# Kernel tuning notes

Hardware: AMD Instinct MI355X
Metric: run time of the kernel (lower is better)

Reference implementation:

```python
import jax, jax.numpy as jnp
import numpy as np

NEG_INF = -1.0e9
LEAKY_SLOPE = 0.2


def setup_inputs() -> dict:
    key = jax.random.key(0)
    k_h, k_w, k_wb, k_a, k_ab, k_m = jax.random.split(key, 6)
    B, S, N, F_in, F_out = 4, 256, 128, 128, 128
    h = jax.random.normal(k_h, (B, S, N, F_in), dtype=jnp.float32)
    # Linear(in_features, out_features): W_w [F_in, F_out], W_b [F_out]
    lim_w = 1.0 / np.sqrt(F_in)
    W_w = jax.random.uniform(k_w, (F_in, F_out), jnp.float32, -lim_w, lim_w)
    W_b = jax.random.uniform(k_wb, (F_out,), jnp.float32, -lim_w, lim_w)
    # Linear(2*F_out, 1): split the weight into a1 (acts on Wh_i) and a2 (acts on Wh_j)
    lim_a = 1.0 / np.sqrt(2 * F_out)
    a_full = jax.random.uniform(k_a, (2 * F_out,), jnp.float32, -lim_a, lim_a)
    a1, a2 = a_full[:F_out], a_full[F_out:]
    a_b = jax.random.uniform(k_ab, (), jnp.float32, -lim_a, lim_a)
    adj_mask = jax.random.randint(k_m, (N, N), 0, 2, dtype=jnp.int32)
    return {"h": h, "W_w": W_w, "W_b": W_b, "a1": a1, "a2": a2,
            "a_b": a_b, "adj_mask": adj_mask}


def reference(h, W_w, W_b, a1, a2, a_b, adj_mask):
    # h: [B, S, N, F_in]
    Wh = jnp.einsum('bsnf,fg->bsng', h, W_w) + W_b          # [B,S,N,F_out]
    # e_ij = leakyrelu(a . [Wh_i ; Wh_j] + b) = leakyrelu(f1_i + f2_j + b)
    f1 = jnp.einsum('bsng,g->bsn', Wh, a1)                   # row term
    f2 = jnp.einsum('bsng,g->bsn', Wh, a2)                   # col term
    e = jax.nn.leaky_relu(f1[..., :, None] + f2[..., None, :] + a_b,
                          negative_slope=LEAKY_SLOPE)        # [B,S,N,N]
    e = jnp.where(adj_mask == 0, NEG_INF, e)
    attention = jax.nn.softmax(e, axis=-1)
    # dropout is identity in eval mode (deterministic reference)
    h_prime = jnp.einsum('bsij,bsjg->bsig', attention, Wh)   # [B,S,N,F_out]
    return jax.nn.elu(h_prime)
```

## Files before the change

kernel.cpp:

```cpp
#include <hip/hip_runtime.h>
#include <hip/hip_bf16.h>
#include <cmath>

namespace {

typedef __attribute__((ext_vector_type(8))) short bf16x8;
typedef __attribute__((ext_vector_type(4))) float f32x4;

constexpr float kNegInf = -1000000000.0f;
constexpr float kSlope  = 0.2f;
constexpr float kLog2e  = 1.44269504088896340736f;

__device__ __forceinline__ unsigned short f2bf(float x) {
  unsigned int u = __float_as_uint(x);
  u = (u + 0x7FFFu + ((u >> 16) & 1u)) >> 16;
  return (unsigned short)u;
}
__device__ __forceinline__ unsigned int f2bf2(float a, float b) {
  __hip_bfloat162 t = __float22bfloat162_rn(float2{a, b});
  union { __hip_bfloat162 h; unsigned int u; } c;
  c.h = t;
  return c.u;
}
__device__ __forceinline__ float exp2_hw(float x) {
#if __has_builtin(__builtin_amdgcn_exp2f)
  return __builtin_amdgcn_exp2f(x);
#else
  float r;
  asm("v_exp_f32 %0, %1\n\ts_nop 1" : "=v"(r) : "v"(x));
  return r;
#endif
}


__global__ void prep1(const float* __restrict__ Ww, const float* __restrict__ Wb,
                      const float* __restrict__ a1v, const float* __restrict__ a2v,
                      float* __restrict__ wa1, float* __restrict__ wa2,
                      float* __restrict__ ba) {
  const int k = threadIdx.x;
  if (k < 128) {
    float s1 = 0.f, s2 = 0.f;
    for (int g = 0; g < 128; ++g) {
      const float w = Ww[k * 128 + g];
      s1 = fmaf(w, a1v[g], s1);
      s2 = fmaf(w, a2v[g], s2);
    }
    wa1[k] = s1 * kLog2e;
    wa2[k] = s2 * kLog2e;
  }
  if (k == 128) {
    float s1 = 0.f, s2 = 0.f;
    for (int g = 0; g < 128; ++g) {
      s1 = fmaf(Wb[g], a1v[g], s1);
      s2 = fmaf(Wb[g], a2v[g], s2);
    }
    ba[0] = s1 * kLog2e;
    ba[1] = s2 * kLog2e;
  }
}

__global__ void prep2(const float* __restrict__ Ww, const int* __restrict__ adj,
                      const float* __restrict__ wa1, const float* __restrict__ wa2,
                      unsigned short* __restrict__ wf, unsigned int* __restrict__ adjp) {
  const int tid = blockIdx.x * 256 + threadIdx.x;
  if (tid < 18432) {
    const int j = tid & 7, l = (tid >> 3) & 63, kc = (tid >> 9) & 3, g = tid >> 11;
    const int k = kc * 32 + ((l >> 4) << 3) + j;
    const int c = l & 15;
    float x;
    if (g < 8) x = Ww[k * 128 + g * 16 + c];
    else       x = (c == 0) ? wa1[k] : (c == 1) ? wa2[k] : 0.f;
    wf[tid] = f2bf(x);
  }
  if (tid < 512) {
    const int row = tid >> 2, wd = tid & 3;
    const int* ap = adj + row * 128 + wd * 32;
    unsigned int bits = 0u;
#pragma unroll
    for (int b = 0; b < 32; ++b) bits |= (ap[b] != 0 ? (1u << b) : 0u);
    adjp[tid] = bits;
  }
}

struct SMemA {
  unsigned short Whs[8][4][64][8];
  float f1s[128];
  float f2s[128];
  unsigned int adjs[512];
};
union SMemU {
  SMemA a;
  float stage[4][16][132];
};

__global__ __launch_bounds__(256, 4) void gat_mfma(
    const float* __restrict__ h,
    const float* __restrict__ Wb,
    const float* __restrict__ abp,
    const unsigned short* __restrict__ wf,
    const unsigned int* __restrict__ adjp,
    const float* __restrict__ ba,
    float* __restrict__ out) {
  __shared__ SMemU smu;
  SMemA& sm = smu.a;
  const int t    = threadIdx.x;
  const int lane = t & 63;
  const int w    = t >> 6;
  const int lr   = lane & 15;
  const int lg   = lane >> 4;
  const int bs   = blockIdx.x;
  const float ab2 = abp[0] * kLog2e;

  *(uint2*)(sm.adjs + t * 2) = *(const uint2*)(adjp + t * 2);

  const float* hblk = h + (size_t)bs * 16384;
  const int R0 = w * 32;

  bf16x8 ha[2][4];
#pragma unroll
  for (int rt = 0; rt < 2; ++rt)
#pragma unroll
    for (int kc = 0; kc < 4; ++kc) {
      const float* p = hblk + (R0 + rt * 16 + lr) * 128 + kc * 32 + lg * 8;
      f32x4 v0 = *(const f32x4*)p;
      f32x4 v1 = *(const f32x4*)(p + 4);
      union { bf16x8 v; unsigned int u[4]; } pk;
      pk.u[0] = f2bf2(v0[0], v0[1]);
      pk.u[1] = f2bf2(v0[2], v0[3]);
      pk.u[2] = f2bf2(v1[0], v1[1]);
      pk.u[3] = f2bf2(v1[2], v1[3]);
      ha[rt][kc] = pk.v;
    }

  f32x4 acc[2][9];
#pragma unroll
  for (int rt = 0; rt < 2; ++rt)
#pragma unroll
    for (int g = 0; g < 9; ++g) acc[rt][g] = (f32x4){0.f, 0.f, 0.f, 0.f};

#pragma unroll
  for (int g = 0; g < 9; ++g)
#pragma unroll
    for (int kc = 0; kc < 4; ++kc) {
      const bf16x8 bh = *(const bf16x8*)(wf + ((g * 4 + kc) * 64 + lane) * 8);
      acc[0][g] = __builtin_amdgcn_mfma_f32_16x16x32_bf16(ha[0][kc], bh, acc[0][g], 0, 0, 0);
      acc[1][g] = __builtin_amdgcn_mfma_f32_16x16x32_bf16(ha[1][kc], bh, acc[1][g], 0, 0, 0);
    }

  float wbc[8];
#pragma unroll
  for (int g = 0; g < 8; ++g) wbc[g] = Wb[g * 16 + lr];
  const float ba1 = ba[0], ba2 = ba[1];

#pragma unroll
  for (int rt = 0; rt < 2; ++rt) {
#pragma unroll
    for (int r = 0; r < 4; ++r) {
#pragma unroll
      for (int g = 0; g < 8; ++g) acc[rt][g][r] += wbc[g];
      const int row = R0 + rt * 16 + lg * 4 + r;
      if (lr == 0)      sm.f1s[row] = acc[rt][8][r] + ba1;
      else if (lr == 1) sm.f2s[row] = acc[rt][8][r] + ba2;
    }
#pragma unroll
    for (int g = 0; g < 8; ++g) {
      const unsigned int plo = f2bf2(acc[rt][g][0], acc[rt][g][1]);
      const unsigned int phi = f2bf2(acc[rt][g][2], acc[rt][g][3]);
      const int lp = (2 * rt + (lg >> 1)) * 16 + lr;
      const int jb = (lg & 1) * 4;
      *(uint2*)(&sm.Whs[g][w][lp][jb]) = make_uint2(plo, phi);
    }
  }
  __syncthreads();

  bf16x8 af[2][4];
  float s0 = 0.f, s1 = 0.f;
  const float f1i0 = sm.f1s[R0 + lr] + ab2;
  const float f1i1 = sm.f1s[R0 + 16 + lr] + ab2;
  const int rq0 = (R0 + lr) * 4, rq1 = (R0 + 16 + lr) * 4;
#pragma unroll
  for (int kc = 0; kc < 4; ++kc) {
    const f32x4 fv0 = *(const f32x4*)(&sm.f2s[kc * 32 + lg * 8]);
    const f32x4 fv1 = *(const f32x4*)(&sm.f2s[kc * 32 + lg * 8 + 4]);
    const unsigned int aw0 = sm.adjs[rq0 + kc];
    const unsigned int aw1 = sm.adjs[rq1 + kc];
    union { bf16x8 v; unsigned int u[4]; } pk0, pk1;
#pragma unroll
    for (int qq = 0; qq < 4; ++qq) {
      float e0[2], e1[2];
#pragma unroll
      for (int hh = 0; hh < 2; ++hh) {
        const int q = qq * 2 + hh;
        const float fj = (q < 4) ? fv0[q] : fv1[q - 4];
        const unsigned int bit = 1u << (lg * 8 + q);
        float x0 = f1i0 + fj;
        x0 = x0 >= 0.f ? x0 : kSlope * x0;
        x0 = (aw0 & bit) ? x0 : kNegInf;
        e0[hh] = exp2_hw(x0);
        float x1 = f1i1 + fj;
        x1 = x1 >= 0.f ? x1 : kSlope * x1;
        x1 = (aw1 & bit) ? x1 : kNegInf;
        e1[hh] = exp2_hw(x1);
      }
      const unsigned int u0 = f2bf2(e0[0], e0[1]);
      const unsigned int u1 = f2bf2(e1[0], e1[1]);
      pk0.u[qq] = u0;
      pk1.u[qq] = u1;
      s0 += __uint_as_float(u0 << 16) + __uint_as_float(u0 & 0xffff0000u);
      s1 += __uint_as_float(u1 << 16) + __uint_as_float(u1 & 0xffff0000u);
    }
    af[0][kc] = pk0.v;
    af[1][kc] = pk1.v;
  }
  s0 += __shfl_xor(s0, 16);
  s0 += __shfl_xor(s0, 32);
  s1 += __shfl_xor(s1, 16);
  s1 += __shfl_xor(s1, 32);
  float rs[2] = {s0, s1};

  f32x4 acc2[2][8];
#pragma unroll
  for (int rt = 0; rt < 2; ++rt)
#pragma unroll
    for (int g = 0; g < 8; ++g) acc2[rt][g] = (f32x4){0.f, 0.f, 0.f, 0.f};

#pragma unroll
  for (int g = 0; g < 8; ++g)
#pragma unroll
    for (int kc = 0; kc < 4; ++kc) {
      const bf16x8 bw = *(const bf16x8*)(&sm.Whs[g][kc][lane][0]);
      acc2[0][g] = __builtin_amdgcn_mfma_f32_16x16x32_bf16(af[0][kc], bw, acc2[0][g], 0, 0, 0);
      acc2[1][g] = __builtin_amdgcn_mfma_f32_16x16x32_bf16(af[1][kc], bw, acc2[1][g], 0, 0, 0);
    }
  __syncthreads();

  float* oblk = out + (size_t)bs * 16384;
#pragma unroll
  for (int rt = 0; rt < 2; ++rt) {
    float inv[4];
#pragma unroll
    for (int r = 0; r < 4; ++r) {
      const float lsum = __shfl(rs[rt], (lane & 48) | (lg * 4 + r));
      inv[r] = __builtin_amdgcn_rcpf(lsum);
    }
#pragma unroll
    for (int r = 0; r < 4; ++r)
#pragma unroll
      for (int g = 0; g < 8; ++g) {
        float v = acc2[rt][g][r] * inv[r];
        v = v > 0.f ? v : __expf(v) - 1.0f;
        smu.stage[w][lg * 4 + r][g * 16 + lr] = v;
      }
#pragma unroll
    for (int sstep = 0; sstep < 8; ++sstep) {
      const int row16 = ((sstep & 1) << 3) + (lane >> 3);
      const int cd    = ((sstep >> 1) << 5) + ((lane & 7) << 2);
      f32x4 vv = *(const f32x4*)(&smu.stage[w][row16][cd]);
      *(f32x4*)(oblk + (size_t)(R0 + rt * 16 + row16) * 128 + cd) = vv;
    }
  }
}

}

extern "C" void kernel_launch(void* const* d_in, const int* in_sizes, int n_in,
                              void* d_out, int out_size, void* d_ws, size_t ws_size,
                              hipStream_t stream) {
  const float* h   = (const float*)d_in[0];
  const float* Ww  = (const float*)d_in[1];
  const float* Wb  = (const float*)d_in[2];
  const float* a1v = (const float*)d_in[3];
  const float* a2v = (const float*)d_in[4];
  const float* ab  = (const float*)d_in[5];
  const int*   adj = (const int*)d_in[6];
  float* out = (float*)d_out;

  unsigned short* wf   = (unsigned short*)d_ws;
  unsigned int*   adjp = (unsigned int*)((char*)d_ws + 36864);
  float*          wa1  = (float*)((char*)d_ws + 38912);
  float*          wa2  = (float*)((char*)d_ws + 39424);
  float*          ba   = (float*)((char*)d_ws + 39936);

  hipLaunchKernelGGL(prep1, dim3(1), dim3(256), 0, stream, Ww, Wb, a1v, a2v, wa1, wa2, ba);
  hipLaunchKernelGGL(prep2, dim3(72), dim3(256), 0, stream, Ww, adj, wa1, wa2, wf, adjp);

  const int BS = in_sizes[0] / 16384;
  hipLaunchKernelGGL(gat_mfma, dim3(BS), dim3(256), 0, stream,
                     h, Wb, ab, wf, adjp, ba, out);
}
```

Baseline: 47.83 us.

## Split fused GAT kernel into separate GEMM and attention kernels via workspace

Splits the single fused kernel into two. The first computes Wh in bf16 plus the f1/f2 row and column terms and writes them to a global workspace. The second reads them back to do the masked softmax, the aggregation MFMA and the ELU. This drops the mid-kernel barrier and the large LDS footprint, which could raise occupancy. The cost is an extra launch and a global round trip of about 2 MB of Wh. The fused path is kept as a fallback when the workspace is too small.

```diff
diff --git a/kernel.cpp b/kernel.cpp
--- a/kernel.cpp
+++ b/kernel.cpp
@@ -32,6 +32,8 @@
 #endif
 }
 
+constexpr size_t kOffF  = 40960;
+constexpr size_t kOffWh = 1089536;
 
 __global__ void prep1(const float* __restrict__ Ww, const float* __restrict__ Wb,
                       const float* __restrict__ a1v, const float* __restrict__ a2v,
@@ -82,37 +84,13 @@
   }
 }
 
-struct SMemA {
-  unsigned short Whs[8][4][64][8];
-  float f1s[128];
-  float f2s[128];
-  unsigned int adjs[512];
-};
-union SMemU {
-  SMemA a;
-  float stage[4][16][132];
-};
-
-__global__ __launch_bounds__(256, 4) void gat_mfma(
-    const float* __restrict__ h,
-    const float* __restrict__ Wb,
-    const float* __restrict__ abp,
-    const unsigned short* __restrict__ wf,
-    const unsigned int* __restrict__ adjp,
-    const float* __restrict__ ba,
-    float* __restrict__ out) {
-  __shared__ SMemU smu;
-  SMemA& sm = smu.a;
-  const int t    = threadIdx.x;
-  const int lane = t & 63;
-  const int w    = t >> 6;
-  const int lr   = lane & 15;
-  const int lg   = lane >> 4;
-  const int bs   = blockIdx.x;
-  const float ab2 = abp[0] * kLog2e;
-
-  *(uint2*)(sm.adjs + t * 2) = *(const uint2*)(adjp + t * 2);
-
+__global__ __launch_bounds__(256, 4) void gat_gemm1(
+    const float* __restrict__ h, const float* __restrict__ Wb,
+    const unsigned short* __restrict__ wf, const float* __restrict__ ba,
+    unsigned short* __restrict__ wsWh, float* __restrict__ wsF) {
+  const int t = threadIdx.x, lane = t & 63, w = t >> 6;
+  const int lr = lane & 15, lg = lane >> 4;
+  const int bs = blockIdx.x;
   const float* hblk = h + (size_t)bs * 16384;
   const int R0 = w * 32;
 
@@ -151,6 +129,8 @@
 #pragma unroll
   for (int g = 0; g < 8; ++g) wbc[g] = Wb[g * 16 + lr];
   const float ba1 = ba[0], ba2 = ba[1];
+  unsigned short* whb = wsWh + (size_t)bs * 16384;
+  float* fb = wsF + bs * 256;
 
 #pragma unroll
   for (int rt = 0; rt < 2; ++rt) {
@@ -159,8 +139,8 @@
 #pragma unroll
       for (int g = 0; g < 8; ++g) acc[rt][g][r] += wbc[g];
       const int row = R0 + rt * 16 + lg * 4 + r;
-      if (lr == 0)      sm.f1s[row] = acc[rt][8][r] + ba1;
-      else if (lr == 1) sm.f2s[row] = acc[rt][8][r] + ba2;
+      if (lr == 0)      fb[row]       = acc[rt][8][r] + ba1;
+      else if (lr == 1) fb[128 + row] = acc[rt][8][r] + ba2;
     }
 #pragma unroll
     for (int g = 0; g < 8; ++g) {
@@ -168,22 +148,35 @@
       const unsigned int phi = f2bf2(acc[rt][g][2], acc[rt][g][3]);
       const int lp = (2 * rt + (lg >> 1)) * 16 + lr;
       const int jb = (lg & 1) * 4;
-      *(uint2*)(&sm.Whs[g][w][lp][jb]) = make_uint2(plo, phi);
-    }
-  }
-  __syncthreads();
+      *(uint2*)(whb + ((g * 4 + w) * 64 + lp) * 8 + jb) = make_uint2(plo, phi);
+    }
+  }
+}
+
+__global__ __launch_bounds__(256, 4) void gat_attn(
+    const unsigned short* __restrict__ wsWh, const float* __restrict__ wsF,
+    const unsigned int* __restrict__ adjp, const float* __restrict__ abp,
+    float* __restrict__ out) {
+  __shared__ float stage[4][16][132];
+  const int t = threadIdx.x, lane = t & 63, w = t >> 6;
+  const int lr = lane & 15, lg = lane >> 4;
+  const int bs = blockIdx.x;
+  const float ab2 = abp[0] * kLog2e;
+  const float* fb = wsF + bs * 256;
+  const unsigned short* whb = wsWh + (size_t)bs * 16384;
+  const int R0 = w * 32;
 
   bf16x8 af[2][4];
   float s0 = 0.f, s1 = 0.f;
-  const float f1i0 = sm.f1s[R0 + lr] + ab2;
-  const float f1i1 = sm.f1s[R0 + 16 + lr] + ab2;
+  const float f1i0 = fb[R0 + lr] + ab2;
+  const float f1i1 = fb[R0 + 16 + lr] + ab2;
   const int rq0 = (R0 + lr) * 4, rq1 = (R0 + 16 + lr) * 4;
 #pragma unroll
   for (int kc = 0; kc < 4; ++kc) {
-    const f32x4 fv0 = *(const f32x4*)(&sm.f2s[kc * 32 + lg * 8]);
-    const f32x4 fv1 = *(const f32x4*)(&sm.f2s[kc * 32 + lg * 8 + 4]);
-    const unsigned int aw0 = sm.adjs[rq0 + kc];
-    const unsigned int aw1 = sm.adjs[rq1 + kc];
+    const f32x4 fv0 = *(const f32x4*)(fb + 128 + kc * 32 + lg * 8);
+    const f32x4 fv1 = *(const f32x4*)(fb + 128 + kc * 32 + lg * 8 + 4);
+    const unsigned int aw0 = adjp[rq0 + kc];
+    const unsigned int aw1 = adjp[rq1 + kc];
     union { bf16x8 v; unsigned int u[4]; } pk0, pk1;
 #pragma unroll
     for (int qq = 0; qq < 4; ++qq) {
@@ -228,6 +221,178 @@
   for (int g = 0; g < 8; ++g)
 #pragma unroll
     for (int kc = 0; kc < 4; ++kc) {
+      const bf16x8 bw = *(const bf16x8*)(whb + ((g * 4 + kc) * 64 + lane) * 8);
+      acc2[0][g] = __builtin_amdgcn_mfma_f32_16x16x32_bf16(af[0][kc], bw, acc2[0][g], 0, 0, 0);
+      acc2[1][g] = __builtin_amdgcn_mfma_f32_16x16x32_bf16(af[1][kc], bw, acc2[1][g], 0, 0, 0);
+    }
+
+  float* oblk = out + (size_t)bs * 16384;
+#pragma unroll
+  for (int rt = 0; rt < 2; ++rt) {
+    float inv[4];
+#pragma unroll
+    for (int r = 0; r < 4; ++r) {
+      const float lsum = __shfl(rs[rt], (lane & 48) | (lg * 4 + r));
+      inv[r] = __builtin_amdgcn_rcpf(lsum);
+    }
+#pragma unroll
+    for (int r = 0; r < 4; ++r)
+#pragma unroll
+      for (int g = 0; g < 8; ++g) {
+        float v = acc2[rt][g][r] * inv[r];
+        v = v > 0.f ? v : __expf(v) - 1.0f;
+        stage[w][lg * 4 + r][g * 16 + lr] = v;
+      }
+#pragma unroll
+    for (int sstep = 0; sstep < 8; ++sstep) {
+      const int row16 = ((sstep & 1) << 3) + (lane >> 3);
+      const int cd    = ((sstep >> 1) << 5) + ((lane & 7) << 2);
+      f32x4 vv = *(const f32x4*)(&stage[w][row16][cd]);
+      *(f32x4*)(oblk + (size_t)(R0 + rt * 16 + row16) * 128 + cd) = vv;
+    }
+  }
+}
+
+struct SMemA {
+  unsigned short Whs[8][4][64][8];
+  float f1s[128];
+  float f2s[128];
+  unsigned int adjs[512];
+};
+union SMemU {
+  SMemA a;
+  float stage[4][16][132];
+};
+
+__global__ __launch_bounds__(256, 4) void gat_mfma(
+    const float* __restrict__ h, const float* __restrict__ Wb,
+    const float* __restrict__ abp, const unsigned short* __restrict__ wf,
+    const unsigned int* __restrict__ adjp, const float* __restrict__ ba,
+    float* __restrict__ out) {
+  __shared__ SMemU smu;
+  SMemA& sm = smu.a;
+  const int t = threadIdx.x, lane = t & 63, w = t >> 6;
+  const int lr = lane & 15, lg = lane >> 4;
+  const int bs = blockIdx.x;
+  const float ab2 = abp[0] * kLog2e;
+
+  *(uint2*)(sm.adjs + t * 2) = *(const uint2*)(adjp + t * 2);
+
+  const float* hblk = h + (size_t)bs * 16384;
+  const int R0 = w * 32;
+
+  bf16x8 ha[2][4];
+#pragma unroll
+  for (int rt = 0; rt < 2; ++rt)
+#pragma unroll
+    for (int kc = 0; kc < 4; ++kc) {
+      const float* p = hblk + (R0 + rt * 16 + lr) * 128 + kc * 32 + lg * 8;
+      f32x4 v0 = *(const f32x4*)p;
+      f32x4 v1 = *(const f32x4*)(p + 4);
+      union { bf16x8 v; unsigned int u[4]; } pk;
+      pk.u[0] = f2bf2(v0[0], v0[1]);
+      pk.u[1] = f2bf2(v0[2], v0[3]);
+      pk.u[2] = f2bf2(v1[0], v1[1]);
+      pk.u[3] = f2bf2(v1[2], v1[3]);
+      ha[rt][kc] = pk.v;
+    }
+
+  f32x4 acc[2][9];
+#pragma unroll
+  for (int rt = 0; rt < 2; ++rt)
+#pragma unroll
+    for (int g = 0; g < 9; ++g) acc[rt][g] = (f32x4){0.f, 0.f, 0.f, 0.f};
+
+#pragma unroll
+  for (int g = 0; g < 9; ++g)
+#pragma unroll
+    for (int kc = 0; kc < 4; ++kc) {
+      const bf16x8 bh = *(const bf16x8*)(wf + ((g * 4 + kc) * 64 + lane) * 8);
+      acc[0][g] = __builtin_amdgcn_mfma_f32_16x16x32_bf16(ha[0][kc], bh, acc[0][g], 0, 0, 0);
+      acc[1][g] = __builtin_amdgcn_mfma_f32_16x16x32_bf16(ha[1][kc], bh, acc[1][g], 0, 0, 0);
+    }
+
+  float wbc[8];
+#pragma unroll
+  for (int g = 0; g < 8; ++g) wbc[g] = Wb[g * 16 + lr];
+  const float ba1 = ba[0], ba2 = ba[1];
+
+#pragma unroll
+  for (int rt = 0; rt < 2; ++rt) {
+#pragma unroll
+    for (int r = 0; r < 4; ++r) {
+#pragma unroll
+      for (int g = 0; g < 8; ++g) acc[rt][g][r] += wbc[g];
+      const int row = R0 + rt * 16 + lg * 4 + r;
+      if (lr == 0)      sm.f1s[row] = acc[rt][8][r] + ba1;
+      else if (lr == 1) sm.f2s[row] = acc[rt][8][r] + ba2;
+    }
+#pragma unroll
+    for (int g = 0; g < 8; ++g) {
+      const unsigned int plo = f2bf2(acc[rt][g][0], acc[rt][g][1]);
+      const unsigned int phi = f2bf2(acc[rt][g][2], acc[rt][g][3]);
+      const int lp = (2 * rt + (lg >> 1)) * 16 + lr;
+      const int jb = (lg & 1) * 4;
+      *(uint2*)(&sm.Whs[g][w][lp][jb]) = make_uint2(plo, phi);
+    }
+  }
+  __syncthreads();
+
+  bf16x8 af[2][4];
+  float s0 = 0.f, s1 = 0.f;
+  const float f1i0 = sm.f1s[R0 + lr] + ab2;
+  const float f1i1 = sm.f1s[R0 + 16 + lr] + ab2;
+  const int rq0 = (R0 + lr) * 4, rq1 = (R0 + 16 + lr) * 4;
+#pragma unroll
+  for (int kc = 0; kc < 4; ++kc) {
+    const f32x4 fv0 = *(const f32x4*)(&sm.f2s[kc * 32 + lg * 8]);
+    const f32x4 fv1 = *(const f32x4*)(&sm.f2s[kc * 32 + lg * 8 + 4]);
+    const unsigned int aw0 = sm.adjs[rq0 + kc];
+    const unsigned int aw1 = sm.adjs[rq1 + kc];
+    union { bf16x8 v; unsigned int u[4]; } pk0, pk1;
+#pragma unroll
+    for (int qq = 0; qq < 4; ++qq) {
+      float e0[2], e1[2];
+#pragma unroll
+      for (int hh = 0; hh < 2; ++hh) {
+        const int q = qq * 2 + hh;
+        const float fj = (q < 4) ? fv0[q] : fv1[q - 4];
+        const unsigned int bit = 1u << (lg * 8 + q);
+        float x0 = f1i0 + fj;
+        x0 = x0 >= 0.f ? x0 : kSlope * x0;
+        x0 = (aw0 & bit) ? x0 : kNegInf;
+        e0[hh] = exp2_hw(x0);
+        float x1 = f1i1 + fj;
+        x1 = x1 >= 0.f ? x1 : kSlope * x1;
+        x1 = (aw1 & bit) ? x1 : kNegInf;
+        e1[hh] = exp2_hw(x1);
+      }
+      const unsigned int u0 = f2bf2(e0[0], e0[1]);
+      const unsigned int u1 = f2bf2(e1[0], e1[1]);
+      pk0.u[qq] = u0;
+      pk1.u[qq] = u1;
+      s0 += __uint_as_float(u0 << 16) + __uint_as_float(u0 & 0xffff0000u);
+      s1 += __uint_as_float(u1 << 16) + __uint_as_float(u1 & 0xffff0000u);
+    }
+    af[0][kc] = pk0.v;
+    af[1][kc] = pk1.v;
+  }
+  s0 += __shfl_xor(s0, 16);
+  s0 += __shfl_xor(s0, 32);
+  s1 += __shfl_xor(s1, 16);
+  s1 += __shfl_xor(s1, 32);
+  float rs[2] = {s0, s1};
+
+  f32x4 acc2[2][8];
+#pragma unroll
+  for (int rt = 0; rt < 2; ++rt)
+#pragma unroll
+    for (int g = 0; g < 8; ++g) acc2[rt][g] = (f32x4){0.f, 0.f, 0.f, 0.f};
+
+#pragma unroll
+  for (int g = 0; g < 8; ++g)
+#pragma unroll
+    for (int kc = 0; kc < 4; ++kc) {
       const bf16x8 bw = *(const bf16x8*)(&sm.Whs[g][kc][lane][0]);
       acc2[0][g] = __builtin_amdgcn_mfma_f32_16x16x32_bf16(af[0][kc], bw, acc2[0][g], 0, 0, 0);
       acc2[1][g] = __builtin_amdgcn_mfma_f32_16x16x32_bf16(af[1][kc], bw, acc2[1][g], 0, 0, 0);
@@ -281,10 +446,18 @@
   float*          wa2  = (float*)((char*)d_ws + 39424);
   float*          ba   = (float*)((char*)d_ws + 39936);
 
+  const int BS = in_sizes[0] / 16384;
+  const size_t need = kOffWh + (size_t)BS * 16384 * sizeof(unsigned short);
+
   hipLaunchKernelGGL(prep1, dim3(1), dim3(256), 0, stream, Ww, Wb, a1v, a2v, wa1, wa2, ba);
   hipLaunchKernelGGL(prep2, dim3(72), dim3(256), 0, stream, Ww, adj, wa1, wa2, wf, adjp);
 
-  const int BS = in_sizes[0] / 16384;
-  hipLaunchKernelGGL(gat_mfma, dim3(BS), dim3(256), 0, stream,
-                     h, Wb, ab, wf, adjp, ba, out);
-}
+  if (ws_size >= need) {
+    float*          wsF  = (float*)((char*)d_ws + kOffF);
+    unsigned short* wsWh = (unsigned short*)((char*)d_ws + kOffWh);
+    hipLaunchKernelGGL(gat_gemm1, dim3(BS), dim3(256), 0, stream, h, Wb, wf, ba, wsWh, wsF);
+    hipLaunchKernelGGL(gat_attn, dim3(BS), dim3(256), 0, stream, wsWh, wsF, adjp, ab, out);
+  } else {
+    hipLaunchKernelGGL(gat_mfma, dim3(BS), dim3(256), 0, stream, h, Wb, ab, wf, adjp, ba, out);
+  }
+}
```

Measured after the change: 54.70 us. +14.4%, slower.

## Process two graph slices per block with register prefetch of next h tile

Applied to the files above, without the earlier changes.

Each block now handles two (b,s) slices in sequence and loads the next slice's h tile into registers while the current slice's MFMA work runs. This is meant to hide global load latency and amortize per-block setup such as the adjacency and bias loads. The stage buffer is no longer unioned with the other shared arrays, so shared memory per block grows. Launch bounds drop to two blocks per CU, the grid is halved to 512 blocks, and the 16 prefetched f32x4 registers raise register pressure.

```diff
diff --git a/kernel.cpp b/kernel.cpp
--- a/kernel.cpp
+++ b/kernel.cpp
@@ -82,181 +82,209 @@
   }
 }
 
-struct SMemA {
+struct SMem {
   unsigned short Whs[8][4][64][8];
   float f1s[128];
   float f2s[128];
   unsigned int adjs[512];
-};
-union SMemU {
-  SMemA a;
   float stage[4][16][132];
 };
 
-__global__ __launch_bounds__(256, 4) void gat_mfma(
+__global__ __launch_bounds__(256, 2) void gat_fused2(
     const float* __restrict__ h,
     const float* __restrict__ Wb,
     const float* __restrict__ abp,
     const unsigned short* __restrict__ wf,
     const unsigned int* __restrict__ adjp,
     const float* __restrict__ ba,
-    float* __restrict__ out) {
-  __shared__ SMemU smu;
-  SMemA& sm = smu.a;
+    float* __restrict__ out,
+    int BS) {
+  __shared__ SMem sm;
   const int t    = threadIdx.x;
   const int lane = t & 63;
   const int w    = t >> 6;
   const int lr   = lane & 15;
   const int lg   = lane >> 4;
-  const int bs   = blockIdx.x;
+  const int R0   = w * 32;
   const float ab2 = abp[0] * kLog2e;
+  const float ba1 = ba[0], ba2v = ba[1];
+
+  float wbc[8];
+#pragma unroll
+  for (int g = 0; g < 8; ++g) wbc[g] = Wb[g * 16 + lr];
 
   *(uint2*)(sm.adjs + t * 2) = *(const uint2*)(adjp + t * 2);
 
-  const float* hblk = h + (size_t)bs * 16384;
-  const int R0 = w * 32;
-
-  bf16x8 ha[2][4];
-#pragma unroll
-  for (int rt = 0; rt < 2; ++rt)
+  constexpr int NB = 2;
+  const int bs0 = blockIdx.x * NB;
+
+  f32x4 pre[16];
+  {
+    const float* hb = h + (size_t)bs0 * 16384;
+#pragma unroll
+    for (int rt = 0; rt < 2; ++rt)
+#pragma unroll
+      for (int kc = 0; kc < 4; ++kc) {
+        const float* p = hb + (R0 + rt * 16 + lr) * 128 + kc * 32 + lg * 8;
+        pre[(rt * 4 + kc) * 2]     = *(const f32x4*)p;
+        pre[(rt * 4 + kc) * 2 + 1] = *(const f32x4*)(p + 4);
+      }
+  }
+
+#pragma unroll
+  for (int it = 0; it < NB; ++it) {
+    const int bs = bs0 + it;
+    if (bs >= BS) break;
+
+    bf16x8 ha[2][4];
+#pragma unroll
+    for (int rt = 0; rt < 2; ++rt)
+#pragma unroll
+      for (int kc = 0; kc < 4; ++kc) {
+        const f32x4 v0 = pre[(rt * 4 + kc) * 2];
+        const f32x4 v1 = pre[(rt * 4 + kc) * 2 + 1];
+        union { bf16x8 v; unsigned int u[4]; } pk;
+        pk.u[0] = f2bf2(v0[0], v0[1]);
+        pk.u[1] = f2bf2(v0[2], v0[3]);
+        pk.u[2] = f2bf2(v1[0], v1[1]);
+        pk.u[3] = f2bf2(v1[2], v1[3]);
+        ha[rt][kc] = pk.v;
+      }
+
+    if (it + 1 < NB && bs + 1 < BS) {
+      const float* hb = h + (size_t)(bs + 1) * 16384;
+#pragma unroll
+      for (int rt = 0; rt < 2; ++rt)
+#pragma unroll
+        for (int kc = 0; kc < 4; ++kc) {
+          const float* p = hb + (R0 + rt * 16 + lr) * 128 + kc * 32 + lg * 8;
+          pre[(rt * 4 + kc) * 2]     = *(const f32x4*)p;
+          pre[(rt * 4 + kc) * 2 + 1] = *(const f32x4*)(p + 4);
+        }
+    }
+
+    f32x4 acc[2][9];
+#pragma unroll
+    for (int rt = 0; rt < 2; ++rt)
+#pragma unroll
+      for (int g = 0; g < 9; ++g) acc[rt][g] = (f32x4){0.f, 0.f, 0.f, 0.f};
+
+#pragma unroll
+    for (int g = 0; g < 9; ++g)
+#pragma unroll
+      for (int kc = 0; kc < 4; ++kc) {
+        const bf16x8 bh = *(const bf16x8*)(wf + ((g * 4 + kc) * 64 + lane) * 8);
+        acc[0][g] = __builtin_amdgcn_mfma_f32_16x16x32_bf16(ha[0][kc], bh, acc[0][g], 0, 0, 0);
+        acc[1][g] = __builtin_amdgcn_mfma_f32_16x16x32_bf16(ha[1][kc], bh, acc[1][g], 0, 0, 0);
+      }
+
+    __syncthreads();
+
+#pragma unroll
+    for (int rt = 0; rt < 2; ++rt) {
+#pragma unroll
+      for (int r = 0; r < 4; ++r) {
+#pragma unroll
+        for (int g = 0; g < 8; ++g) acc[rt][g][r] += wbc[g];
+        const int row = R0 + rt * 16 + lg * 4 + r;
+        if (lr == 0)      sm.f1s[row] = acc[rt][8][r] + ba1;
+        else if (lr == 1) sm.f2s[row] = acc[rt][8][r] + ba2v;
+      }
+#pragma unroll
+      for (int g = 0; g < 8; ++g) {
+        const unsigned int plo = f2bf2(acc[rt][g][0], acc[rt][g][1]);
+        const unsigned int phi = f2bf2(acc[rt][g][2], acc[rt][g][3]);
+        const int lp = (2 * rt + (lg >> 1)) * 16 + lr;
+        const int jb = (lg & 1) * 4;
+        *(uint2*)(&sm.Whs[g][w][lp][jb]) = make_uint2(plo, phi);
+      }
+    }
+    __syncthreads();
+
+    bf16x8 af[2][4];
+    float s0 = 0.f, s1 = 0.f;
+    const float f1i0 = sm.f1s[R0 + lr] + ab2;
+    const float f1i1 = sm.f1s[R0 + 16 + lr] + ab2;
+    const int rq0 = (R0 + lr) * 4, rq1 = (R0 + 16 + lr) * 4;
 #pragma unroll
     for (int kc = 0; kc < 4; ++kc) {
-      const float* p = hblk + (R0 + rt * 16 + lr) * 128 + kc * 32 + lg * 8;
-      f32x4 v0 = *(const f32x4*)p;
-      f32x4 v1 = *(const f32x4*)(p + 4);
-      union { bf16x8 v; unsigned int u[4]; } pk;
-      pk.u[0] = f2bf2(v0[0], v0[1]);
-      pk.u[1] = f2bf2(v0[2], v0[3]);
-      pk.u[2] = f2bf2(v1[0], v1[1]);
-      pk.u[3] = f2bf2(v1[2], v1[3]);
-      ha[rt][kc] = pk.v;
-    }
-
-  f32x4 acc[2][9];
-#pragma unroll
-  for (int rt = 0; rt < 2; ++rt)
-#pragma unroll
-    for (int g = 0; g < 9; ++g) acc[rt][g] = (f32x4){0.f, 0.f, 0.f, 0.f};
-
-#pragma unroll
-  for (int g = 0; g < 9; ++g)
-#pragma unroll
-    for (int kc = 0; kc < 4; ++kc) {
-      const bf16x8 bh = *(const bf16x8*)(wf + ((g * 4 + kc) * 64 + lane) * 8);
-      acc[0][g] = __builtin_amdgcn_mfma_f32_16x16x32_bf16(ha[0][kc], bh, acc[0][g], 0, 0, 0);
-      acc[1][g] = __builtin_amdgcn_mfma_f32_16x16x32_bf16(ha[1][kc], bh, acc[1][g], 0, 0, 0);
-    }
-
-  float wbc[8];
-#pragma unroll
-  for (int g = 0; g < 8; ++g) wbc[g] = Wb[g * 16 + lr];
-  const float ba1 = ba[0], ba2 = ba[1];
-
-#pragma unroll
-  for (int rt = 0; rt < 2; ++rt) {
-#pragma unroll
-    for (int r = 0; r < 4; ++r) {
-#pragma unroll
-      for (int g = 0; g < 8; ++g) acc[rt][g][r] += wbc[g];
-      const int row = R0 + rt * 16 + lg * 4 + r;
-      if (lr == 0)      sm.f1s[row] = acc[rt][8][r] + ba1;
-      else if (lr == 1) sm.f2s[row] = acc[rt][8][r] + ba2;
-    }
-#pragma unroll
-    for (int g = 0; g < 8; ++g) {
-      const unsigned int plo = f2bf2(acc[rt][g][0], acc[rt][g][1]);
-      const unsigned int phi = f2bf2(acc[rt][g][2], acc[rt][g][3]);
-      const int lp = (2 * rt + (lg >> 1)) * 16 + lr;
-      const int jb = (lg & 1) * 4;
-      *(uint2*)(&sm.Whs[g][w][lp][jb]) = make_uint2(plo, phi);
-    }
-  }
-  __syncthreads();
-
-  bf16x8 af[2][4];
-  float s0 = 0.f, s1 = 0.f;
-  const float f1i0 = sm.f1s[R0 + lr] + ab2;
-  const float f1i1 = sm.f1s[R0 + 16 + lr] + ab2;
-  const int rq0 = (R0 + lr) * 4, rq1 = (R0 + 16 + lr) * 4;
-#pragma unroll
-  for (int kc = 0; kc < 4; ++kc) {
-    const f32x4 fv0 = *(const f32x4*)(&sm.f2s[kc * 32 + lg * 8]);
-    const f32x4 fv1 = *(const f32x4*)(&sm.f2s[kc * 32 + lg * 8 + 4]);
-    const unsigned int aw0 = sm.adjs[rq0 + kc];
-    const unsigned int aw1 = sm.adjs[rq1 + kc];
-    union { bf16x8 v; unsigned int u[4]; } pk0, pk1;
-#pragma unroll
-    for (int qq = 0; qq < 4; ++qq) {
-      float e0[2], e1[2];
-#pragma unroll
-      for (int hh = 0; hh < 2; ++hh) {
-        const int q = qq * 2 + hh;
-        const float fj = (q < 4) ? fv0[q] : fv1[q - 4];
-        const unsigned int bit = 1u << (lg * 8 + q);
-        float x0 = f1i0 + fj;
-        x0 = x0 >= 0.f ? x0 : kSlope * x0;
-        x0 = (aw0 & bit) ? x0 : kNegInf;
-        e0[hh] = exp2_hw(x0);
-        float x1 = f1i1 + fj;
-        x1 = x1 >= 0.f ? x1 : kSlope * x1;
-        x1 = (aw1 & bit) ? x1 : kNegInf;
-        e1[hh] = exp2_hw(x1);
-      }
-      const unsigned int u0 = f2bf2(e0[0], e0[1]);
-      const unsigned int u1 = f2bf2(e1[0], e1[1]);
-      pk0.u[qq] = u0;
-      pk1.u[qq] = u1;
-      s0 += __uint_as_float(u0 << 16) + __uint_as_float(u0 & 0xffff0000u);
-      s1 += __uint_as_float(u1 << 16) + __uint_as_float(u1 & 0xffff0000u);
-    }
-    af[0][kc] = pk0.v;
-    af[1][kc] = pk1.v;
-  }
-  s0 += __shfl_xor(s0, 16);
-  s0 += __shfl_xor(s0, 32);
-  s1 += __shfl_xor(s1, 16);
-  s1 += __shfl_xor(s1, 32);
-  float rs[2] = {s0, s1};
-
-  f32x4 acc2[2][8];
-#pragma unroll
-  for (int rt = 0; rt < 2; ++rt)
-#pragma unroll
-    for (int g = 0; g < 8; ++g) acc2[rt][g] = (f32x4){0.f, 0.f, 0.f, 0.f};
-
-#pragma unroll
-  for (int g = 0; g < 8; ++g)
-#pragma unroll
-    for (int kc = 0; kc < 4; ++kc) {
-      const bf16x8 bw = *(const bf16x8*)(&sm.Whs[g][kc][lane][0]);
-      acc2[0][g] = __builtin_amdgcn_mfma_f32_16x16x32_bf16(af[0][kc], bw, acc2[0][g], 0, 0, 0);
-      acc2[1][g] = __builtin_amdgcn_mfma_f32_16x16x32_bf16(af[1][kc], bw, acc2[1][g], 0, 0, 0);
-    }
-  __syncthreads();
-
-  float* oblk = out + (size_t)bs * 16384;
-#pragma unroll
-  for (int rt = 0; rt < 2; ++rt) {
-    float inv[4];
-#pragma unroll
-    for (int r = 0; r < 4; ++r) {
-      const float lsum = __shfl(rs[rt], (lane & 48) | (lg * 4 + r));
-      inv[r] = __builtin_amdgcn_rcpf(lsum);
-    }
-#pragma unroll
-    for (int r = 0; r < 4; ++r)
-#pragma unroll
-      for (int g = 0; g < 8; ++g) {
-        float v = acc2[rt][g][r] * inv[r];
-        v = v > 0.f ? v : __expf(v) - 1.0f;
-        smu.stage[w][lg * 4 + r][g * 16 + lr] = v;
-      }
-#pragma unroll
-    for (int sstep = 0; sstep < 8; ++sstep) {
-      const int row16 = ((sstep & 1) << 3) + (lane >> 3);
-      const int cd    = ((sstep >> 1) << 5) + ((lane & 7) << 2);
-      f32x4 vv = *(const f32x4*)(&smu.stage[w][row16][cd]);
-      *(f32x4*)(oblk + (size_t)(R0 + rt * 16 + row16) * 128 + cd) = vv;
+      const f32x4 fv0 = *(const f32x4*)(&sm.f2s[kc * 32 + lg * 8]);
+      const f32x4 fv1 = *(const f32x4*)(&sm.f2s[kc * 32 + lg * 8 + 4]);
+      const unsigned int aw0 = sm.adjs[rq0 + kc];
+      const unsigned int aw1 = sm.adjs[rq1 + kc];
+      union { bf16x8 v; unsigned int u[4]; } pk0, pk1;
+#pragma unroll
+      for (int qq = 0; qq < 4; ++qq) {
+        float e0[2], e1[2];
+#pragma unroll
+        for (int hh = 0; hh < 2; ++hh) {
+          const int q = qq * 2 + hh;
+          const float fj = (q < 4) ? fv0[q] : fv1[q - 4];
+          const unsigned int bit = 1u << (lg * 8 + q);
+          float x0 = f1i0 + fj;
+          x0 = x0 >= 0.f ? x0 : kSlope * x0;
+          x0 = (aw0 & bit) ? x0 : kNegInf;
+          e0[hh] = exp2_hw(x0);
+          float x1 = f1i1 + fj;
+          x1 = x1 >= 0.f ? x1 : kSlope * x1;
+          x1 = (aw1 & bit) ? x1 : kNegInf;
+          e1[hh] = exp2_hw(x1);
+        }
+        const unsigned int u0 = f2bf2(e0[0], e0[1]);
+        const unsigned int u1 = f2bf2(e1[0], e1[1]);
+        pk0.u[qq] = u0;
+        pk1.u[qq] = u1;
+        s0 += __uint_as_float(u0 << 16) + __uint_as_float(u0 & 0xffff0000u);
+        s1 += __uint_as_float(u1 << 16) + __uint_as_float(u1 & 0xffff0000u);
+      }
+      af[0][kc] = pk0.v;
+      af[1][kc] = pk1.v;
+    }
+    s0 += __shfl_xor(s0, 16);
+    s0 += __shfl_xor(s0, 32);
+    s1 += __shfl_xor(s1, 16);
+    s1 += __shfl_xor(s1, 32);
+    float rs[2] = {s0, s1};
+
+    f32x4 acc2[2][8];
+#pragma unroll
+    for (int rt = 0; rt < 2; ++rt)
+#pragma unroll
+      for (int g = 0; g < 8; ++g) acc2[rt][g] = (f32x4){0.f, 0.f, 0.f, 0.f};
+
+#pragma unroll
+    for (int g = 0; g < 8; ++g)
+#pragma unroll
+      for (int kc = 0; kc < 4; ++kc) {
+        const bf16x8 bw = *(const bf16x8*)(&sm.Whs[g][kc][lane][0]);
+        acc2[0][g] = __builtin_amdgcn_mfma_f32_16x16x32_bf16(af[0][kc], bw, acc2[0][g], 0, 0, 0);
+        acc2[1][g] = __builtin_amdgcn_mfma_f32_16x16x32_bf16(af[1][kc], bw, acc2[1][g], 0, 0, 0);
+      }
+
+    float* oblk = out + (size_t)bs * 16384;
+#pragma unroll
+    for (int rt = 0; rt < 2; ++rt) {
+      float inv[4];
+#pragma unroll
+      for (int r = 0; r < 4; ++r) {
+        const float lsum = __shfl(rs[rt], (lane & 48) | (lg * 4 + r));
+        inv[r] = __builtin_amdgcn_rcpf(lsum);
+      }
+#pragma unroll
+      for (int r = 0; r < 4; ++r)
+#pragma unroll
+        for (int g = 0; g < 8; ++g) {
+          float v = acc2[rt][g][r] * inv[r];
+          v = v > 0.f ? v : __expf(v) - 1.0f;
+          sm.stage[w][lg * 4 + r][g * 16 + lr] = v;
+        }
+#pragma unroll
+      for (int sstep = 0; sstep < 8; ++sstep) {
+        const int row16 = ((sstep & 1) << 3) + (lane >> 3);
+        const int cd    = ((sstep >> 1) << 5) + ((lane & 7) << 2);
+        f32x4 vv = *(const f32x4*)(&sm.stage[w][row16][cd]);
+        *(f32x4*)(oblk + (size_t)(R0 + rt * 16 + row16) * 128 + cd) = vv;
+      }
     }
   }
 }
@@ -285,6 +313,7 @@
   hipLaunchKernelGGL(prep2, dim3(72), dim3(256), 0, stream, Ww, adj, wa1, wa2, wf, adjp);
 
   const int BS = in_sizes[0] / 16384;
-  hipLaunchKernelGGL(gat_mfma, dim3(BS), dim3(256), 0, stream,
-                     h, Wb, ab, wf, adjp, ba, out);
-}
+  const int grid = (BS + 1) / 2;
+  hipLaunchKernelGGL(gat_fused2, dim3(grid), dim3(256), 0, stream,
+                     h, Wb, ab, wf, adjp, ba, out, BS);
+}
```

New measurement: 51.73 us. 1.08x slower.
